# Kernel optimization log

Measured on AMD Instinct MI355X. Metric: run time of the kernel, lower is better.

Reference implementation:

```python
import jax, jax.numpy as jnp
import numpy as np


def _conv(x, w, b, stride=1, pad=0):
    # x: NCHW, w: OIHW (torch layout)
    y = jax.lax.conv_general_dilated(
        x, w, (stride, stride), [(pad, pad), (pad, pad)],
        dimension_numbers=('NCHW', 'OIHW', 'NCHW'))
    return y + b[None, :, None, None]


def _convT(x, w, b):
    # torch ConvTranspose2d(k=4, stride=2, padding=1); w: [Cin, Cout, 4, 4]
    wf = jnp.flip(w, (2, 3)).transpose(1, 0, 2, 3)  # -> OIHW
    y = jax.lax.conv_general_dilated(
        x, wf, (1, 1), [(2, 2), (2, 2)], lhs_dilation=(2, 2),
        dimension_numbers=('NCHW', 'OIHW', 'NCHW'))
    return y + b[None, :, None, None]


def _quantize(z, embed):
    # z: [B,H,W,D], embed: [D,K]  (eval-mode _Quantize: no EMA update)
    f = z.reshape(-1, z.shape[-1])
    dist = (f * f).sum(1, keepdims=True) - 2.0 * (f @ embed) + (embed * embed).sum(0, keepdims=True)
    ind = jnp.argmin(dist, axis=1)
    q = embed.T[ind].reshape(z.shape)
    diff = jnp.mean((jax.lax.stop_gradient(q) - z) ** 2)[None]
    q = z + jax.lax.stop_gradient(q - z)  # straight-through
    return q, diff, ind.reshape(z.shape[:-1])


def setup_inputs() -> dict:
    key = jax.random.key(0)
    ks = jax.random.split(key, 22)
    s = 0.02
    r = lambda k, sh, sc=s: jax.random.normal(k, sh, jnp.float32) * sc
    z = lambda sh: jnp.zeros(sh, jnp.float32)
    return {
        'x': jax.random.normal(ks[0], (16, 3, 256, 256), jnp.float32),
        # encoder_bottom: two stride-2 4x4 convs, 3->128->128 (256->64)
        'wb1': r(ks[1], (128, 3, 4, 4)), 'bb1': z(128),
        'wb2': r(ks[2], (128, 128, 4, 4)), 'bb2': z(128),
        # encoder_top: one stride-2 4x4 conv, 128->128 (64->32)
        'wt1': r(ks[3], (128, 128, 4, 4)), 'bt1': z(128),
        # quantize_conv_t: 1x1, 128->64
        'wqt': r(ks[4], (64, 128, 1, 1)), 'bqt': z(64),
        'embed_t': jax.random.normal(ks[5], (64, 512), jnp.float32),
        # decoder_top: convT 64->64 (32->64)
        'wdt': r(ks[6], (64, 64, 4, 4)), 'bdt': z(64),
        # quantize_conv_b: 1x1, 192->64
        'wqb': r(ks[7], (64, 192, 1, 1)), 'bqb': z(64),
        'embed_b': jax.random.normal(ks[8], (64, 512), jnp.float32),
        # upsample_t: convT 64->64 (32->64)
        'wup': r(ks[9], (64, 64, 4, 4)), 'bup': z(64),
        # decoder_bottom: convT 128->64 (64->128), convT 64->3 (128->256)
        'wd1': r(ks[10], (128, 64, 4, 4)), 'bd1': z(64),
        'wd2': r(ks[11], (64, 3, 4, 4)), 'bd2': z(3),
    }


def reference(x, wb1, bb1, wb2, bb2, wt1, bt1, wqt, bqt, embed_t,
              wdt, bdt, wqb, bqb, embed_b, wup, bup, wd1, bd1, wd2, bd2):
    # ----- encode -----
    enc_b = jax.nn.relu(_conv(x, wb1, bb1, stride=2, pad=1))          # [B,128,128,128]
    enc_b = jax.nn.relu(_conv(enc_b, wb2, bb2, stride=2, pad=1))      # [B,128,64,64]
    enc_t = jax.nn.relu(_conv(enc_b, wt1, bt1, stride=2, pad=1))      # [B,128,32,32]

    qt = _conv(enc_t, wqt, bqt).transpose(0, 2, 3, 1)                 # [B,32,32,64]
    quant_t, diff_t, id_t = _quantize(qt, embed_t)
    quant_t = quant_t.transpose(0, 3, 1, 2)                           # [B,64,32,32]

    dec_t = _convT(quant_t, wdt, bdt)                                 # [B,64,64,64]
    enc_cat = jnp.concatenate([dec_t, enc_b], axis=1)                 # [B,192,64,64]

    qb = _conv(enc_cat, wqb, bqb).transpose(0, 2, 3, 1)               # [B,64,64,64]
    quant_b, diff_b, id_b = _quantize(qb, embed_b)
    quant_b = quant_b.transpose(0, 3, 1, 2)                           # [B,64,64,64]

    loss_commit = diff_t + diff_b                                     # [1]

    # ----- decode -----
    up_t = _convT(quant_t, wup, bup)                                  # [B,64,64,64]
    quant = jnp.concatenate([up_t, quant_b], axis=1)                  # [B,128,64,64]
    h = jax.nn.relu(_convT(quant, wd1, bd1))                          # [B,64,128,128]
    x_hat = _convT(h, wd2, bd2)                                       # [B,3,256,256]

    return x_hat, quant_t, quant_b, loss_commit, id_t, id_b
```

## Files before the change

### kernel.cpp

```cpp
#include <hip/hip_runtime.h>

#define TPB 256

typedef __attribute__((ext_vector_type(4))) float f32x4;
typedef __attribute__((ext_vector_type(8))) short bf16x8;

__global__ void wtrans_kernel(const float* __restrict__ src, float* __restrict__ dst,
                              int CIN, int COUT, int taps, int iohw) {
    int idx = blockIdx.x * TPB + threadIdx.x;
    int tot = CIN * COUT * taps;
    if (idx >= tot) return;
    int co = idx % COUT;
    int ci = (idx / COUT) % CIN;
    int tap = idx / (COUT * CIN);
    float v = iohw ? src[(ci * COUT + co) * taps + tap]
                   : src[(co * CIN + ci) * taps + tap];
    dst[idx] = v;
}

__device__ __forceinline__ unsigned bf16_rne(float v) {
    unsigned u = __float_as_uint(v);
    return (u + 0x7FFFu + ((u >> 16) & 1u)) >> 16;
}

__global__ void wtrans_bf16_kernel(const float* __restrict__ src, short* __restrict__ dst,
                                   int CIN, int COUT, int taps, int iohw, int PL) {
    int idx = blockIdx.x * TPB + threadIdx.x;
    int tot = CIN * COUT * taps;
    if (idx >= tot) return;
    int ci = idx % CIN;
    int co = (idx / CIN) % COUT;
    int tap = idx / (CIN * COUT);
    float v = iohw ? src[(ci * COUT + co) * taps + tap]
                   : src[(co * CIN + ci) * taps + tap];
    unsigned h = bf16_rne(v);
    float rem = v - __uint_as_float(h << 16);
    unsigned l = bf16_rne(rem);
    dst[idx] = (short)h;
    dst[idx + PL] = (short)l;
}

__global__ void wtrans_wd2_kernel(const float* __restrict__ src, short* __restrict__ dst) {
    int idx = blockIdx.x * TPB + threadIdx.x;
    if (idx >= 16384) return;
    int ci  = idx & 63;
    int co  = (idx >> 6) & 15;
    int tap = (idx >> 10) & 3;
    int cls = idx >> 12;
    int py = cls >> 1, px = cls & 1;
    int jj = tap >> 1, ii = tap & 1;
    int ky = (1 - py) + 2 * jj;
    int kx = (1 - px) + 2 * ii;
    float v = (co < 3) ? src[(ci * 3 + co) * 16 + ky * 4 + kx] : 0.f;
    dst[idx] = (short)bf16_rne(v);
}

__global__ void etrans_kernel(const float* __restrict__ et, const float* __restrict__ eb,
                              short* __restrict__ ETt, short* __restrict__ ETb) {
    int idx = blockIdx.x * TPB + threadIdx.x;
    if (idx >= 65536) return;
    const float* src = (idx < 32768) ? et : eb;
    short* dst = (idx < 32768) ? ETt : ETb;
    int i = idx & 32767;
    int k = i & 63;
    int n = i >> 6;
    float v = src[k * 512 + n];
    unsigned h = bf16_rne(v);
    float rem = v - __uint_as_float(h << 16);
    dst[i] = (short)h;
    dst[i + 32768] = (short)bf16_rne(rem);
}

__device__ __forceinline__ void cvt_split2(float a, float b, unsigned& hw, unsigned& lw) {
    unsigned ha = bf16_rne(a), hb = bf16_rne(b);
    float ra = a - __uint_as_float(ha << 16);
    float rb = b - __uint_as_float(hb << 16);
    hw = ha | (hb << 16);
    lw = bf16_rne(ra) | (bf16_rne(rb) << 16);
}
__device__ __forceinline__ unsigned cvt_pk(float a, float b) {
    return bf16_rne(a) | (bf16_rne(b) << 16);
}

template<int MODE, int CIN, int COUT, int SPLIT, int RELU,
         int IH, int IW, int OH, int OW, int R, int INBF, int OUTB>
__global__ __launch_bounds__(256) void mfma_conv(
    const void* __restrict__ inv, const short* __restrict__ Wb,
    const float* __restrict__ bias, float* __restrict__ outp,
    short* __restrict__ outb) {
    constexpr int TAPS = (MODE == 0) ? 16 : 4;
    constexpr int CW = (MODE == 0) ? OW : OW / 2;
    constexpr int CH = (MODE == 0) ? OH : OH / 2;
    constexpr int NCH = CIN / 32;
    constexpr int MTc = (COUT == 128) ? 4 : 2;
    constexpr long PL = (long)TAPS * COUT * CIN;
    constexpr long APL_IN  = 16L * IH * IW * CIN;
    constexpr long APL_OUT = 16L * OH * OW * COUT;

    __shared__ short Ah[128 * 40];
    __shared__ short Al[SPLIT ? 128 * 40 : 8];
    __shared__ short Bh[COUT * 40];
    __shared__ short Bl[SPLIT ? COUT * 40 : 8];

    int bx = blockIdx.x;
    int ry = 0, rx = 0;
    if (MODE == 1) { int c = bx & 3; ry = c >> 1; rx = c & 1; bx >>= 2; }
    const int y0 = (bx % (CH / R)) * R;
    const int n  = bx / (CH / R);

    const int tid = threadIdx.x;
    const int p  = tid >> 1;
    const int ak = (tid & 1) * 16;
    const int rr = p / CW, xx = p % CW;
    constexpr int BPT = (COUT * 32) / 256;
    constexpr int TPRB = 32 / BPT;
    const int bco = tid / TPRB;
    const int bk  = (tid % TPRB) * BPT;
    const int lane = tid & 63, wv = tid >> 6;
    const int quad = lane >> 4, l16 = lane & 15;
    const int mbase = (COUT == 128) ? (wv & 1) * 64 : wv * 32;
    const int nbase = (COUT == 128) ? (wv >> 1) * 64 : 0;

    f32x4 acc[MTc][4];
#pragma unroll
    for (int mt = 0; mt < MTc; ++mt)
#pragma unroll
        for (int nt = 0; nt < 4; ++nt) acc[mt][nt] = f32x4{0.f, 0.f, 0.f, 0.f};

#pragma unroll 1
    for (int tap = 0; tap < TAPS; ++tap) {
        int iy, ix, wt;
        if (MODE == 0) {
            int ky = tap >> 2, kx = tap & 3;
            iy = 2 * (y0 + rr) - 1 + ky;
            ix = 2 * xx - 1 + kx;
            wt = tap;
        } else {
            int jj = tap >> 1, ii = tap & 1;
            iy = (y0 + rr) + ry - jj;
            ix = xx + rx - ii;
            wt = ((1 - ry) + 2 * jj) * 4 + ((1 - rx) + 2 * ii);
        }
        const bool av = (iy >= 0) && (iy < IH) && (ix >= 0) && (ix < IW);
        const long abase = ((long)(n * IH + iy) * IW + ix) * CIN + ak;
        const short* wrh = Wb + ((long)wt * COUT + bco) * CIN + bk;

#pragma unroll 1
        for (int cb = 0; cb < NCH; ++cb) {
            __syncthreads();
            if constexpr (INBF) {
                const short* sb = (const short*)inv + abase + cb * 32;
                uint4 h0, h1;
                if (av) { h0 = *(const uint4*)sb; h1 = *(const uint4*)(sb + 8); }
                else { h0 = make_uint4(0,0,0,0); h1 = h0; }
                *(uint4*)&Ah[p * 40 + ak]     = h0;
                *(uint4*)&Ah[p * 40 + ak + 8] = h1;
                if constexpr (SPLIT) {
                    uint4 l0, l1;
                    if (av) { l0 = *(const uint4*)(sb + APL_IN); l1 = *(const uint4*)(sb + APL_IN + 8); }
                    else { l0 = make_uint4(0,0,0,0); l1 = l0; }
                    *(uint4*)&Al[p * 40 + ak]     = l0;
                    *(uint4*)&Al[p * 40 + ak + 8] = l1;
                }
            } else {
                const float* sp = (const float*)inv + abase + cb * 32;
                float4 f[4];
                if (av) {
#pragma unroll
                    for (int i = 0; i < 4; ++i) f[i] = *(const float4*)(sp + 4 * i);
                } else {
#pragma unroll
                    for (int i = 0; i < 4; ++i) { f[i].x = 0.f; f[i].y = 0.f; f[i].z = 0.f; f[i].w = 0.f; }
                }
                if constexpr (SPLIT) {
                    unsigned hw[8], lw[8];
#pragma unroll
                    for (int i = 0; i < 4; ++i) {
                        cvt_split2(f[i].x, f[i].y, hw[2 * i], lw[2 * i]);
                        cvt_split2(f[i].z, f[i].w, hw[2 * i + 1], lw[2 * i + 1]);
                    }
                    *(uint4*)&Ah[p * 40 + ak]     = make_uint4(hw[0], hw[1], hw[2], hw[3]);
                    *(uint4*)&Ah[p * 40 + ak + 8] = make_uint4(hw[4], hw[5], hw[6], hw[7]);
                    *(uint4*)&Al[p * 40 + ak]     = make_uint4(lw[0], lw[1], lw[2], lw[3]);
                    *(uint4*)&Al[p * 40 + ak + 8] = make_uint4(lw[4], lw[5], lw[6], lw[7]);
                } else {
                    unsigned hw[8];
#pragma unroll
                    for (int i = 0; i < 4; ++i) {
                        hw[2 * i]     = cvt_pk(f[i].x, f[i].y);
                        hw[2 * i + 1] = cvt_pk(f[i].z, f[i].w);
                    }
                    *(uint4*)&Ah[p * 40 + ak]     = make_uint4(hw[0], hw[1], hw[2], hw[3]);
                    *(uint4*)&Ah[p * 40 + ak + 8] = make_uint4(hw[4], hw[5], hw[6], hw[7]);
                }
            }
#pragma unroll
            for (int i = 0; i < BPT / 8; ++i) {
                *(uint4*)&Bh[bco * 40 + bk + 8 * i] = *(const uint4*)(wrh + cb * 32 + 8 * i);
                if constexpr (SPLIT)
                    *(uint4*)&Bl[bco * 40 + bk + 8 * i] = *(const uint4*)(wrh + PL + cb * 32 + 8 * i);
            }
            __syncthreads();
            bf16x8 ahf[MTc], alf[SPLIT ? MTc : 1];
#pragma unroll
            for (int mt = 0; mt < MTc; ++mt) {
                ahf[mt] = *(const bf16x8*)&Ah[(mbase + mt * 16 + l16) * 40 + quad * 8];
                if constexpr (SPLIT)
                    alf[mt] = *(const bf16x8*)&Al[(mbase + mt * 16 + l16) * 40 + quad * 8];
            }
#pragma unroll
            for (int nt = 0; nt < 4; ++nt) {
                bf16x8 bhf = *(const bf16x8*)&Bh[(nbase + nt * 16 + l16) * 40 + quad * 8];
#pragma unroll
                for (int mt = 0; mt < MTc; ++mt)
                    acc[mt][nt] = __builtin_amdgcn_mfma_f32_16x16x32_bf16(ahf[mt], bhf, acc[mt][nt], 0, 0, 0);
                if constexpr (SPLIT) {
                    bf16x8 blf = *(const bf16x8*)&Bl[(nbase + nt * 16 + l16) * 40 + quad * 8];
#pragma unroll
                    for (int mt = 0; mt < MTc; ++mt) {
                        acc[mt][nt] = __builtin_amdgcn_mfma_f32_16x16x32_bf16(alf[mt], bhf, acc[mt][nt], 0, 0, 0);
                        acc[mt][nt] = __builtin_amdgcn_mfma_f32_16x16x32_bf16(ahf[mt], blf, acc[mt][nt], 0, 0, 0);
                    }
                }
            }
        }
    }
#pragma unroll
    for (int mt = 0; mt < MTc; ++mt)
#pragma unroll
        for (int nt = 0; nt < 4; ++nt) {
            int co = nbase + nt * 16 + l16;
            float bv = bias[co];
#pragma unroll
            for (int r = 0; r < 4; ++r) {
                int pl = mbase + mt * 16 + quad * 4 + r;
                int rr2 = pl / CW, x2 = pl % CW;
                int oy, ox;
                if (MODE == 0) { oy = y0 + rr2; ox = x2; }
                else           { oy = 2 * (y0 + rr2) + ry; ox = 2 * x2 + rx; }
                float vv = acc[mt][nt][r] + bv;
                if (RELU) vv = fmaxf(vv, 0.f);
                long oidx = ((long)(n * OH + oy) * OW + ox) * COUT + co;
                if constexpr (OUTB == 0 || OUTB == 1) outp[oidx] = vv;
                if constexpr (OUTB == 1 || OUTB == 3) {
                    unsigned hh = bf16_rne(vv);
                    outb[oidx] = (short)hh;
                    outb[oidx + APL_OUT] = (short)bf16_rne(vv - __uint_as_float(hh << 16));
                }
                if constexpr (OUTB == 2) outb[oidx] = (short)bf16_rne(vv);
            }
        }
}

__global__ __launch_bounds__(256) void convt_final_mfma(
    const short* __restrict__ h, const short* __restrict__ Wc,
    const float* __restrict__ bias, float* __restrict__ out) {
    const int HW = 128;
    __shared__ short HB[3 * 130 * 72];
    __shared__ float Sout[6 * 260];

    const int tid = threadIdx.x;
    const int y = blockIdx.x & 127;
    const int n = blockIdx.x >> 7;
    const int lane = tid & 63, wv = tid >> 6;
    const int quad = lane >> 4, l16 = lane & 15;

    for (int u = tid; u < 780; u += TPB) {
        int row = u >> 1, half = u & 1;
        int hr = row / 130, xc = row % 130;
        int hy = y - 1 + hr, hx = xc - 1;
        bool ok = (hy >= 0 && hy < HW && hx >= 0 && hx < HW);
        const short* sp = h + ((long)(n * HW + hy) * HW + hx) * 64 + half * 32;
        uint4 a0, a1, a2, a3;
        if (ok) {
            a0 = *(const uint4*)sp;       a1 = *(const uint4*)(sp + 8);
            a2 = *(const uint4*)(sp + 16); a3 = *(const uint4*)(sp + 24);
        } else {
            a0 = make_uint4(0,0,0,0); a1 = a0; a2 = a0; a3 = a0;
        }
        short* dp = &HB[row * 72 + half * 32];
        *(uint4*)dp = a0; *(uint4*)(dp + 8) = a1;
        *(uint4*)(dp + 16) = a2; *(uint4*)(dp + 24) = a3;
    }
    __syncthreads();

#pragma unroll 1
    for (int cls = 0; cls < 4; ++cls) {
        const int py = cls >> 1, px = cls & 1;
        bf16x8 Bf[4][2];
#pragma unroll
        for (int tap = 0; tap < 4; ++tap)
#pragma unroll
            for (int cb = 0; cb < 2; ++cb)
                Bf[tap][cb] = *(const bf16x8*)&Wc[((cls * 4 + tap) * 16 + l16) * 64 + cb * 32 + quad * 8];

        f32x4 acc2[2] = { f32x4{0.f,0.f,0.f,0.f}, f32x4{0.f,0.f,0.f,0.f} };
#pragma unroll
        for (int mt = 0; mt < 2; ++mt) {
            const int xp0 = wv * 32 + mt * 16;
#pragma unroll
            for (int tap = 0; tap < 4; ++tap) {
                const int jj = tap >> 1, ii = tap & 1;
                const int hr = py - jj + 1;
                const int rbase = (hr * 130 + xp0 + l16 + px - ii + 1) * 72;
#pragma unroll
                for (int cb = 0; cb < 2; ++cb) {
                    bf16x8 Af = *(const bf16x8*)&HB[rbase + cb * 32 + quad * 8];
                    acc2[mt] = __builtin_amdgcn_mfma_f32_16x16x32_bf16(Af, Bf[tap][cb], acc2[mt], 0, 0, 0);
                }
            }
        }
        if (l16 < 3) {
#pragma unroll
            for (int mt = 0; mt < 2; ++mt)
#pragma unroll
                for (int r = 0; r < 4; ++r) {
                    int xp = wv * 32 + mt * 16 + quad * 4 + r;
                    Sout[(py * 3 + l16) * 260 + 2 * xp + px] = acc2[mt][r];
                }
        }
    }
    __syncthreads();

    for (int u = tid; u < 384; u += TPB) {
        int idx = u * 4;
        int rowi = idx >> 8;
        int xq   = idx & 255;
        int py = rowi / 3, co = rowi % 3;
        float bv = bias[co];
        float4 v = *(const float4*)&Sout[rowi * 260 + xq];
        v.x += bv; v.y += bv; v.z += bv; v.w += bv;
        *(float4*)&out[(((long)(n * 3 + co) * 256) + 2 * y + py) * 256 + xq] = v;
    }
}

__global__ __launch_bounds__(256) void conv1_kernel(
    const float* __restrict__ x, const float* __restrict__ Wt,
    const float* __restrict__ bias, short* __restrict__ outb) {
    const int IH = 256, IW = 256, OH = 128, OW = 128, BM = 64;
    const long APL0 = 16L * 128 * 128 * 128;
    int bx = blockIdx.x;
    int sx = bx & 1;
    int oy = (bx >> 1) & 127;
    int n  = bx >> 8;
    int ox0 = sx * BM;
    __shared__ float Bs[16 * 3 * 128];
    __shared__ float Ts[3 * 4 * 132];
    int tid = threadIdx.x;
    for (int i = tid; i < 6144 / 4; i += TPB)
        ((float4*)Bs)[i] = ((const float4*)Wt)[i];
    int iy0 = 2 * oy - 1;
    for (int idx = tid; idx < 3 * 4 * 130; idx += TPB) {
        int ci = idx / 520; int r = idx % 520;
        int ky = r / 130;   int xx = r % 130;
        int iy = iy0 + ky;  int ix = 2 * ox0 - 1 + xx;
        float v = 0.f;
        if (iy >= 0 && iy < IH && ix >= 0 && ix < IW)
            v = x[((n * 3 + ci) * IH + iy) * IW + ix];
        Ts[(ci * 4 + ky) * 132 + xx] = v;
    }
    __syncthreads();
    int cog = tid & 31, pxg = tid >> 5;
    int co0 = cog * 4, px0 = pxg * 8;
    float acc[8][4];
#pragma unroll
    for (int i = 0; i < 8; ++i)
#pragma unroll
        for (int j = 0; j < 4; ++j) acc[i][j] = 0.f;
#pragma unroll 1
    for (int ky = 0; ky < 4; ++ky)
#pragma unroll 1
        for (int kx = 0; kx < 4; ++kx)
#pragma unroll
            for (int ci = 0; ci < 3; ++ci) {
                float4 b = *(const float4*)&Bs[((ky * 4 + kx) * 3 + ci) * 128 + co0];
                const float* trow = &Ts[(ci * 4 + ky) * 132 + kx];
#pragma unroll
                for (int q = 0; q < 8; ++q) {
                    float a = trow[2 * (px0 + q)];
                    acc[q][0] = fmaf(a, b.x, acc[q][0]);
                    acc[q][1] = fmaf(a, b.y, acc[q][1]);
                    acc[q][2] = fmaf(a, b.z, acc[q][2]);
                    acc[q][3] = fmaf(a, b.w, acc[q][3]);
                }
            }
    float4 bb = *(const float4*)&bias[co0];
#pragma unroll
    for (int q = 0; q < 8; ++q) {
        int ox = ox0 + px0 + q;
        float v0 = fmaxf(acc[q][0] + bb.x, 0.f);
        float v1 = fmaxf(acc[q][1] + bb.y, 0.f);
        float v2 = fmaxf(acc[q][2] + bb.z, 0.f);
        float v3 = fmaxf(acc[q][3] + bb.w, 0.f);
        unsigned h0, l0, h1, l1;
        cvt_split2(v0, v1, h0, l0);
        cvt_split2(v2, v3, h1, l1);
        long pix = ((long)n * OH + oy) * OW + ox;
        *(uint2*)&outb[pix * 128 + co0]        = make_uint2(h0, h1);
        *(uint2*)&outb[APL0 + pix * 128 + co0] = make_uint2(l0, l1);
    }
}

template<int MODE, int CIN, int COUT, int BM, int RELU, int IH, int IW, int OH, int OW>
__global__ __launch_bounds__(256) void conv_gemm(
    const float* __restrict__ in, const float* __restrict__ Wt,
    const float* __restrict__ bias, float* __restrict__ out) {
    constexpr int CHUNK  = 64;
    constexpr int NCH    = CIN / CHUNK;
    constexpr int CO_PER = (COUT == 128) ? 4 : 2;
    constexpr int PX_PER = BM / 8;
    constexpr int TAPS   = (MODE == 0) ? 16 : (MODE == 1 ? 4 : 1);
    __shared__ float As[CHUNK * BM];
    __shared__ float Bs[CHUNK * COUT];
    const int tid = threadIdx.x;
    const int bx  = blockIdx.x;
    int n, oy, ox0 = 0, par = 0;
    if (MODE == 1) {
        par = bx & 1;
        oy  = (bx >> 1) % OH;
        n   = bx / (2 * OH);
    } else {
        constexpr int SPR = OW / BM;
        int s = bx % SPR;
        oy = (bx / SPR) % OH;
        n  = bx / (SPR * OH);
        ox0 = s * BM;
    }
    const int cog = tid & 31;
    const int pxg = tid >> 5;
    const int co0 = cog * CO_PER, px0 = pxg * PX_PER;
    float acc[PX_PER][CO_PER];
#pragma unroll
    for (int q = 0; q < PX_PER; ++q)
#pragma unroll
        for (int j = 0; j < CO_PER; ++j) acc[q][j] = 0.f;
    constexpr int TPX  = 256 / BM;
    constexpr int CIPT = CHUNK / TPX;
    const int spx  = tid / TPX;
    const int sci0 = (tid % TPX) * CIPT;
    const int py   = oy & 1;

#pragma unroll 1
    for (int tap = 0; tap < TAPS; ++tap) {
        int iy, twi, sx;
        if (MODE == 0) {
            int ky = tap >> 2, kx = tap & 3;
            iy  = 2 * oy - 1 + ky;
            sx  = 2 * (ox0 + spx) - 1 + kx;
            twi = tap;
        } else if (MODE == 1) {
            int jj = tap >> 1, ii = tap & 1;
            iy  = ((oy + 1) >> 1) - jj;
            sx  = spx + par - ii;
            twi = ((1 - py) + 2 * jj) * 4 + ((1 - par) + 2 * ii);
        } else {
            iy = oy; sx = ox0 + spx; twi = 0;
        }
        const bool pxv = (iy >= 0) && (iy < IH) && (sx >= 0) && (sx < IW);
        const float* srcp = in + (((long)n * IH + iy) * IW + sx) * CIN + sci0;
#pragma unroll 1
        for (int cb = 0; cb < NCH; ++cb) {
            __syncthreads();
            float4 tmp[CIPT / 4];
#pragma unroll
            for (int t4 = 0; t4 < CIPT / 4; ++t4) {
                if (pxv) tmp[t4] = *(const float4*)(srcp + cb * CHUNK + 4 * t4);
                else { tmp[t4].x = 0.f; tmp[t4].y = 0.f; tmp[t4].z = 0.f; tmp[t4].w = 0.f; }
            }
#pragma unroll
            for (int t4 = 0; t4 < CIPT / 4; ++t4) {
                As[(sci0 + 4 * t4 + 0) * BM + spx] = tmp[t4].x;
                As[(sci0 + 4 * t4 + 1) * BM + spx] = tmp[t4].y;
                As[(sci0 + 4 * t4 + 2) * BM + spx] = tmp[t4].z;
                As[(sci0 + 4 * t4 + 3) * BM + spx] = tmp[t4].w;
            }
            {
                const float4* wsrc = (const float4*)(Wt + ((long)twi * CIN + cb * CHUNK) * COUT);
#pragma unroll
                for (int t4 = 0; t4 < (CHUNK * COUT) / 1024; ++t4)
                    ((float4*)Bs)[tid + 256 * t4] = wsrc[tid + 256 * t4];
            }
            __syncthreads();
#pragma unroll 4
            for (int k = 0; k < CHUNK; ++k) {
                float a[PX_PER];
#pragma unroll
                for (int t4 = 0; t4 < PX_PER / 4; ++t4)
                    *(float4*)&a[4 * t4] = *(const float4*)&As[k * BM + px0 + 4 * t4];
                if constexpr (CO_PER == 4) {
                    float4 b = *(const float4*)&Bs[k * COUT + co0];
#pragma unroll
                    for (int q = 0; q < PX_PER; ++q) {
                        acc[q][0] = fmaf(a[q], b.x, acc[q][0]);
                        acc[q][1] = fmaf(a[q], b.y, acc[q][1]);
                        acc[q][2] = fmaf(a[q], b.z, acc[q][2]);
                        acc[q][3] = fmaf(a[q], b.w, acc[q][3]);
                    }
                } else {
                    float2 b = *(const float2*)&Bs[k * COUT + co0];
#pragma unroll
                    for (int q = 0; q < PX_PER; ++q) {
                        acc[q][0] = fmaf(a[q], b.x, acc[q][0]);
                        acc[q][1] = fmaf(a[q], b.y, acc[q][1]);
                    }
                }
            }
        }
    }
    float bv[CO_PER];
#pragma unroll
    for (int j = 0; j < CO_PER; ++j) bv[j] = bias[co0 + j];
#pragma unroll
    for (int q = 0; q < PX_PER; ++q) {
        int ox = (MODE == 1) ? (par + 2 * (px0 + q)) : (ox0 + px0 + q);
        float* op = out + (((long)n * OH + oy) * OW + ox) * COUT + co0;
        if constexpr (CO_PER == 4) {
            float4 v;
            v.x = acc[q][0] + bv[0]; v.y = acc[q][1] + bv[1];
            v.z = acc[q][2] + bv[2]; v.w = acc[q][3] + bv[3];
            if (RELU) { v.x = fmaxf(v.x, 0.f); v.y = fmaxf(v.y, 0.f);
                        v.z = fmaxf(v.z, 0.f); v.w = fmaxf(v.w, 0.f); }
            *(float4*)op = v;
        } else {
            float2 v;
            v.x = acc[q][0] + bv[0]; v.y = acc[q][1] + bv[1];
            if (RELU) { v.x = fmaxf(v.x, 0.f); v.y = fmaxf(v.y, 0.f); }
            *(float2*)op = v;
        }
    }
}

__global__ void enorm_kernel(const float* __restrict__ et, const float* __restrict__ eb,
                             float* __restrict__ nt, float* __restrict__ nb) {
    int k = blockIdx.x * TPB + threadIdx.x;
    if (k >= 1024) return;
    const float* e = (k < 512) ? et : eb;
    float* o = (k < 512) ? nt : nb;
    int kk = k & 511;
    float s = 0.f;
#pragma unroll 8
    for (int d = 0; d < 64; ++d) { float v = e[d * 512 + kk]; s = fmaf(v, v, s); }
    o[kk] = s;
}

__global__ __launch_bounds__(256) void quantize_mfma(
    const float* __restrict__ f, const short* __restrict__ ET,
    const float* __restrict__ embed, const float* __restrict__ enorm,
    float* __restrict__ qn, float* __restrict__ qc, float* __restrict__ ido,
    float* __restrict__ dsum, int M, int HW) {
    __shared__ short Fh[64 * 72];
    __shared__ short Fl[64 * 72];
    __shared__ float S[64 * 65];
    __shared__ int   KI[64];
    __shared__ float wsum[4];

    const int tid = threadIdx.x;
    const int lane = tid & 63, wv = tid >> 6;
    const int quad = lane >> 4, l16 = lane & 15;
    const int R0 = blockIdx.x * 64;

    {
        int row = tid >> 2;
        int k0 = (tid & 3) * 16;
        const float* sp = f + (long)(R0 + row) * 64 + k0;
        unsigned hw[8], lw[8];
#pragma unroll
        for (int i = 0; i < 4; ++i) {
            float4 p = *(const float4*)(sp + 4 * i);
            cvt_split2(p.x, p.y, hw[2 * i], lw[2 * i]);
            cvt_split2(p.z, p.w, hw[2 * i + 1], lw[2 * i + 1]);
        }
        short* dh = &Fh[row * 72 + k0];
        short* dl = &Fl[row * 72 + k0];
        *(uint4*)(dh)     = make_uint4(hw[0], hw[1], hw[2], hw[3]);
        *(uint4*)(dh + 8) = make_uint4(hw[4], hw[5], hw[6], hw[7]);
        *(uint4*)(dl)     = make_uint4(lw[0], lw[1], lw[2], lw[3]);
        *(uint4*)(dl + 8) = make_uint4(lw[4], lw[5], lw[6], lw[7]);
    }
    __syncthreads();

    const int arow = (wv * 16 + l16) * 72;
    bf16x8 Ah0 = *(const bf16x8*)&Fh[arow + quad * 8];
    bf16x8 Ah1 = *(const bf16x8*)&Fh[arow + 32 + quad * 8];
    bf16x8 Al0 = *(const bf16x8*)&Fl[arow + quad * 8];
    bf16x8 Al1 = *(const bf16x8*)&Fl[arow + 32 + quad * 8];

    float bestv[4];
    int   besti[4];
#pragma unroll
    for (int r = 0; r < 4; ++r) { bestv[r] = 3.4e38f; besti[r] = 0; }

    const short* ETlo = ET + 32768;
#pragma unroll 2
    for (int j = 0; j < 32; ++j) {
        const int nb = (j * 16 + l16) * 64 + quad * 8;
        bf16x8 Bh0 = *(const bf16x8*)(ET + nb);
        bf16x8 Bh1 = *(const bf16x8*)(ET + nb + 32);
        bf16x8 Bl0 = *(const bf16x8*)(ETlo + nb);
        bf16x8 Bl1 = *(const bf16x8*)(ETlo + nb + 32);
        f32x4 acc = f32x4{0.f, 0.f, 0.f, 0.f};
        acc = __builtin_amdgcn_mfma_f32_16x16x32_bf16(Ah0, Bh0, acc, 0, 0, 0);
        acc = __builtin_amdgcn_mfma_f32_16x16x32_bf16(Ah1, Bh1, acc, 0, 0, 0);
        acc = __builtin_amdgcn_mfma_f32_16x16x32_bf16(Al0, Bh0, acc, 0, 0, 0);
        acc = __builtin_amdgcn_mfma_f32_16x16x32_bf16(Al1, Bh1, acc, 0, 0, 0);
        acc = __builtin_amdgcn_mfma_f32_16x16x32_bf16(Ah0, Bl0, acc, 0, 0, 0);
        acc = __builtin_amdgcn_mfma_f32_16x16x32_bf16(Ah1, Bl1, acc, 0, 0, 0);
        float en = enorm[j * 16 + l16];
        int   ni = j * 16 + l16;
#pragma unroll
        for (int r = 0; r < 4; ++r) {
            float s = fmaf(-2.f, acc[r], en);
            if (s < bestv[r]) { bestv[r] = s; besti[r] = ni; }
        }
    }
#pragma unroll
    for (int m = 1; m < 16; m <<= 1) {
#pragma unroll
        for (int r = 0; r < 4; ++r) {
            float ov = __shfl_xor(bestv[r], m);
            int   oi = __shfl_xor(besti[r], m);
            if (ov < bestv[r] || (ov == bestv[r] && oi < besti[r])) {
                bestv[r] = ov; besti[r] = oi;
            }
        }
    }
    if (l16 == 0) {
#pragma unroll
        for (int r = 0; r < 4; ++r) KI[wv * 16 + quad * 4 + r] = besti[r];
    }
    __syncthreads();

    float ddacc = 0.f;
#pragma unroll 1
    for (int r16 = 0; r16 < 16; ++r16) {
        int row = wv * 16 + r16;
        int k = KI[row];
        float ev = embed[lane * 512 + k];
        float fv = f[(long)(R0 + row) * 64 + lane];
        qn[(long)(R0 + row) * 64 + lane] = ev;
        S[row * 65 + lane] = ev;
        float dq = ev - fv;
        ddacc = fmaf(dq, dq, ddacc);
        if (lane == 0) ido[R0 + row] = (float)k;
    }
#pragma unroll
    for (int off = 1; off < 64; off <<= 1) ddacc += __shfl_xor(ddacc, off);
    if (lane == 0) wsum[wv] = ddacc;
    __syncthreads();
    if (tid == 0)
        atomicAdd(dsum, wsum[0] + wsum[1] + wsum[2] + wsum[3]);

    int nn = R0 / HW;
    int rem0 = R0 - nn * HW;
    int px = tid & 63;
    int cg = tid >> 6;
#pragma unroll
    for (int it = 0; it < 16; ++it) {
        int c = cg + 4 * it;
        qc[((long)nn * 64 + c) * HW + rem0 + px] = S[px * 65 + c];
    }
}

__global__ void concat_rec_kernel(const float* __restrict__ a, const short* __restrict__ bh,
                                  float* __restrict__ o, int M) {
    const long PLB = 8388608L;
    int idx = blockIdx.x * TPB + threadIdx.x;
    if (idx >= M * 48) return;
    int row = idx / 48;
    int c4  = (idx - row * 48) * 4;
    float4 v;
    if (c4 < 64) v = *(const float4*)(a + (long)row * 64 + c4);
    else {
        int cc = c4 - 64;
        uint2 h = *(const uint2*)(bh + (long)row * 128 + cc);
        uint2 l = *(const uint2*)(bh + PLB + (long)row * 128 + cc);
        v.x = __uint_as_float(h.x << 16)        + __uint_as_float(l.x << 16);
        v.y = __uint_as_float(h.x & 0xFFFF0000u) + __uint_as_float(l.x & 0xFFFF0000u);
        v.z = __uint_as_float(h.y << 16)        + __uint_as_float(l.y << 16);
        v.w = __uint_as_float(h.y & 0xFFFF0000u) + __uint_as_float(l.y & 0xFFFF0000u);
    }
    *(float4*)(o + (long)row * 192 + c4) = v;
}

__global__ void concat_bf16_kernel(const float* __restrict__ a, const float* __restrict__ b,
                                   short* __restrict__ o, int M) {
    int idx = blockIdx.x * TPB + threadIdx.x;
    if (idx >= M * 32) return;
    int row = idx / 32;
    int c4  = (idx - row * 32) * 4;
    float4 v;
    if (c4 < 64) v = *(const float4*)(a + (long)row * 64 + c4);
    else         v = *(const float4*)(b + (long)row * 64 + (c4 - 64));
    *(uint2*)(o + (long)row * 128 + c4) = make_uint2(cvt_pk(v.x, v.y), cvt_pk(v.z, v.w));
}

__global__ void loss_kernel(const float* __restrict__ sums, float* __restrict__ out) {
    out[0] = sums[0] * (1.f / (16384.f * 64.f)) + sums[1] * (1.f / (65536.f * 64.f));
}

extern "C" void kernel_launch(void* const* d_in, const int* in_sizes, int n_in,
                              void* d_out, int out_size, void* d_ws, size_t ws_size,
                              hipStream_t stream) {
    const float* x   = (const float*)d_in[0];
    const float* wb1 = (const float*)d_in[1];  const float* bb1 = (const float*)d_in[2];
    const float* wb2 = (const float*)d_in[3];  const float* bb2 = (const float*)d_in[4];
    const float* wt1 = (const float*)d_in[5];  const float* bt1 = (const float*)d_in[6];
    const float* wqt = (const float*)d_in[7];  const float* bqt = (const float*)d_in[8];
    const float* embed_t = (const float*)d_in[9];
    const float* wdt = (const float*)d_in[10]; const float* bdt = (const float*)d_in[11];
    const float* wqb = (const float*)d_in[12]; const float* bqb = (const float*)d_in[13];
    const float* embed_b = (const float*)d_in[14];
    const float* wup = (const float*)d_in[15]; const float* bup = (const float*)d_in[16];
    const float* wd1 = (const float*)d_in[17]; const float* bd1 = (const float*)d_in[18];
    const float* wd2 = (const float*)d_in[19]; const float* bd2 = (const float*)d_in[20];
    float* out = (float*)d_out;
    float* ws  = (float*)d_ws;

    float* O_XHAT = out;
    float* O_QT   = out + 3145728;
    float* O_QB   = out + 4194304;
    float* O_LOSS = out + 8388608;
    float* O_IDT  = out + 8388609;
    float* O_IDB  = out + 8404993;

    float* W_WB1 = ws + 0;
    short* WB_WD2 = (short*)(ws + 16384);
    short* ET_T  = (short*)(ws + 32768);
    short* ET_B  = (short*)(ws + 65536);
    float* W_WQT = ws + 532480;
    float* W_WDT = ws + 540672;
    float* W_WQB = ws + 606208;
    float* EN_T  = ws + 818176;
    float* EN_B  = ws + 818688;
    float* SUMS  = ws + 819200;
    short* T1B  = (short*)(ws + 1048576);
    const long BIG = 9437184;
    short* T0B  = (short*)(ws + BIG);
    float* T2   = ws + BIG;
    float* QT   = ws + BIG + 2097152;
    float* QTN  = ws + BIG + 3145728;
    float* DECT = ws + BIG + 4194304;
    float* ECAT = ws + BIG + 8388608;
    float* QB   = ws + BIG + 20971520;
    float* QBN  = ws + BIG + 25165824;
    float* UPT  = ws + BIG + 4194304;
    short* QCATB = (short*)(ws + BIG + 8388608);
    short* HBUFB = (short*)(ws + BIG + 16777216);
    short* WB_BF2 = (short*)(ws + 42991616);
    short* WB_BT1 = (short*)(ws + 43253760);
    short* WB_BD1 = (short*)(ws + 43515904);
    short* WB_BUP = (short*)(ws + 43646976);

    auto wt_launch = [&](const float* src, float* dst, int cin, int cout, int taps, int iohw) {
        int tot = cin * cout * taps;
        wtrans_kernel<<<(tot + TPB - 1) / TPB, TPB, 0, stream>>>(src, dst, cin, cout, taps, iohw);
    };
    auto wtb_launch = [&](const float* src, short* dst, int cin, int cout, int taps, int iohw) {
        int tot = cin * cout * taps;
        wtrans_bf16_kernel<<<(tot + TPB - 1) / TPB, TPB, 0, stream>>>(src, dst, cin, cout, taps, iohw, tot);
    };
    wt_launch(wb1, W_WB1, 3, 128, 16, 0);
    wt_launch(wqt, W_WQT, 128, 64, 1, 0);
    wt_launch(wdt, W_WDT, 64, 64, 16, 1);
    wt_launch(wqb, W_WQB, 192, 64, 1, 0);
    wtrans_wd2_kernel<<<64, TPB, 0, stream>>>(wd2, WB_WD2);
    wtb_launch(wb2, WB_BF2, 128, 128, 16, 0);
    wtb_launch(wt1, WB_BT1, 128, 128, 16, 0);
    wtb_launch(wd1, WB_BD1, 128, 64, 16, 1);
    wtb_launch(wup, WB_BUP, 64, 64, 16, 1);
    enorm_kernel<<<4, TPB, 0, stream>>>(embed_t, embed_b, EN_T, EN_B);
    etrans_kernel<<<256, TPB, 0, stream>>>(embed_t, embed_b, ET_T, ET_B);
    hipError_t e0 = hipMemsetAsync((void*)SUMS, 0, 2 * sizeof(float), stream);
    (void)e0;

    conv1_kernel<<<4096, TPB, 0, stream>>>(x, W_WB1, bb1, T0B);
    mfma_conv<0, 128, 128, 1, 1, 128, 128, 64, 64, 2, 1, 3>
        <<<512, TPB, 0, stream>>>(T0B, WB_BF2, bb2, nullptr, T1B);
    mfma_conv<0, 128, 128, 1, 1, 64, 64, 32, 32, 4, 1, 0>
        <<<128, TPB, 0, stream>>>(T1B, WB_BT1, bt1, T2, nullptr);
    conv_gemm<2, 128, 64, 32, 0, 32, 32, 32, 32><<<512, TPB, 0, stream>>>(T2, W_WQT, bqt, QT);
    quantize_mfma<<<256, TPB, 0, stream>>>(QT, ET_T, embed_t, EN_T, QTN, O_QT, O_IDT, SUMS,
                                           16384, 1024);
    conv_gemm<1, 64, 64, 32, 0, 32, 32, 64, 64><<<2048, TPB, 0, stream>>>(QTN, W_WDT, bdt, DECT);
    concat_rec_kernel<<<12288, TPB, 0, stream>>>(DECT, T1B, ECAT, 65536);
    conv_gemm<2, 192, 64, 64, 0, 64, 64, 64, 64><<<1024, TPB, 0, stream>>>(ECAT, W_WQB, bqb, QB);
    quantize_mfma<<<1024, TPB, 0, stream>>>(QB, ET_B, embed_b, EN_B, QBN, O_QB, O_IDB, SUMS + 1,
                                            65536, 4096);
    mfma_conv<1, 64, 64, 0, 0, 32, 32, 64, 64, 4, 0, 0>
        <<<512, TPB, 0, stream>>>(QTN, WB_BUP, bup, UPT, nullptr);
    concat_bf16_kernel<<<8192, TPB, 0, stream>>>(UPT, QBN, QCATB, 65536);
    mfma_conv<1, 128, 64, 0, 1, 64, 64, 128, 128, 2, 1, 2>
        <<<2048, TPB, 0, stream>>>(QCATB, WB_BD1, bd1, nullptr, HBUFB);
    convt_final_mfma<<<2048, TPB, 0, stream>>>(HBUFB, WB_WD2, bd2, O_XHAT);
    loss_kernel<<<1, 1, 0, stream>>>(SUMS, O_LOSS);

    (void)in_sizes; (void)n_in; (void)out_size; (void)ws_size;
}
```

Measured before the change: 707.5 us.

## Move 1x1 top quantize conv to MFMA and pass bf16 activations between stages

Adds a K-tile size parameter to the MFMA conv so each barrier-protected round covers 64 input channels instead of 32, and a 1x1 mode. The top-encoder conv now writes split-bf16 output, which a new MFMA 1x1 conv consumes in place of the fp32 FMA GEMM. The quantizer also emits bf16 copies of the quantized codes, so upsample and concat read bf16 directly instead of converting fp32. The aim is fewer sync rounds, tensor-core use for the 1x1 conv, and less fp32 traffic, at the cost of more shared memory per block and extra bf16 stores.

New measurement: 730.6 us. 3.3% more time.

```diff
diff --git a/kernel.cpp b/kernel.cpp
--- a/kernel.cpp
+++ b/kernel.cpp
@@ -35,9 +35,8 @@
                    : src[(co * CIN + ci) * taps + tap];
     unsigned h = bf16_rne(v);
     float rem = v - __uint_as_float(h << 16);
-    unsigned l = bf16_rne(rem);
     dst[idx] = (short)h;
-    dst[idx + PL] = (short)l;
+    dst[idx + PL] = (short)bf16_rne(rem);
 }
 
 __global__ void wtrans_wd2_kernel(const float* __restrict__ src, short* __restrict__ dst) {
@@ -83,24 +82,30 @@
 }
 
 template<int MODE, int CIN, int COUT, int SPLIT, int RELU,
-         int IH, int IW, int OH, int OW, int R, int INBF, int OUTB>
+         int IH, int IW, int OH, int OW, int R, int INBF, int OUTB, int KR>
 __global__ __launch_bounds__(256) void mfma_conv(
     const void* __restrict__ inv, const short* __restrict__ Wb,
     const float* __restrict__ bias, float* __restrict__ outp,
     short* __restrict__ outb) {
-    constexpr int TAPS = (MODE == 0) ? 16 : 4;
-    constexpr int CW = (MODE == 0) ? OW : OW / 2;
-    constexpr int CH = (MODE == 0) ? OH : OH / 2;
-    constexpr int NCH = CIN / 32;
+    constexpr int TAPS = (MODE == 0) ? 16 : (MODE == 1 ? 4 : 1);
+    constexpr int CW = (MODE == 1) ? OW / 2 : OW;
+    constexpr int CH = (MODE == 1) ? OH / 2 : OH;
+    constexpr int NRND = CIN / KR;
+    constexpr int KC = KR / 32;
+    constexpr int ST = KR + 8;
     constexpr int MTc = (COUT == 128) ? 4 : 2;
-    constexpr long PL = (long)TAPS * COUT * CIN;
+    constexpr long PLW = (long)TAPS * COUT * CIN;
     constexpr long APL_IN  = 16L * IH * IW * CIN;
     constexpr long APL_OUT = 16L * OH * OW * COUT;
-
-    __shared__ short Ah[128 * 40];
-    __shared__ short Al[SPLIT ? 128 * 40 : 8];
-    __shared__ short Bh[COUT * 40];
-    __shared__ short Bl[SPLIT ? COUT * 40 : 8];
+    constexpr int NU4A = KR / 16;
+    constexpr int TPR  = 256 / COUT;
+    constexpr int SPT  = KR / TPR;
+    constexpr int NU4B = SPT / 8;
+
+    __shared__ short Ah[128 * ST];
+    __shared__ short Al[SPLIT ? 128 * ST : 8];
+    __shared__ short Bh[COUT * ST];
+    __shared__ short Bl[SPLIT ? COUT * ST : 8];
 
     int bx = blockIdx.x;
     int ry = 0, rx = 0;
@@ -109,13 +114,11 @@
     const int n  = bx / (CH / R);
 
     const int tid = threadIdx.x;
-    const int p  = tid >> 1;
-    const int ak = (tid & 1) * 16;
+    const int p   = tid >> 1;
+    const int akb = (tid & 1) * (KR / 2);
     const int rr = p / CW, xx = p % CW;
-    constexpr int BPT = (COUT * 32) / 256;
-    constexpr int TPRB = 32 / BPT;
-    const int bco = tid / TPRB;
-    const int bk  = (tid % TPRB) * BPT;
+    const int bco = tid / TPR;
+    const int bk  = (tid % TPR) * SPT;
     const int lane = tid & 63, wv = tid >> 6;
     const int quad = lane >> 4, l16 = lane & 15;
     const int mbase = (COUT == 128) ? (wv & 1) * 64 : wv * 32;
@@ -135,91 +138,82 @@
             iy = 2 * (y0 + rr) - 1 + ky;
             ix = 2 * xx - 1 + kx;
             wt = tap;
-        } else {
+        } else if (MODE == 1) {
             int jj = tap >> 1, ii = tap & 1;
             iy = (y0 + rr) + ry - jj;
             ix = xx + rx - ii;
             wt = ((1 - ry) + 2 * jj) * 4 + ((1 - rx) + 2 * ii);
-        }
-        const bool av = (iy >= 0) && (iy < IH) && (ix >= 0) && (ix < IW);
-        const long abase = ((long)(n * IH + iy) * IW + ix) * CIN + ak;
-        const short* wrh = Wb + ((long)wt * COUT + bco) * CIN + bk;
+        } else {
+            iy = y0 + rr; ix = xx; wt = 0;
+        }
+        const bool av = (MODE == 2) ||
+                        ((iy >= 0) && (iy < IH) && (ix >= 0) && (ix < IW));
+        const long abase = ((long)(n * IH + iy) * IW + ix) * CIN + akb;
 
 #pragma unroll 1
-        for (int cb = 0; cb < NCH; ++cb) {
+        for (int ko = 0; ko < NRND; ++ko) {
             __syncthreads();
             if constexpr (INBF) {
-                const short* sb = (const short*)inv + abase + cb * 32;
-                uint4 h0, h1;
-                if (av) { h0 = *(const uint4*)sb; h1 = *(const uint4*)(sb + 8); }
-                else { h0 = make_uint4(0,0,0,0); h1 = h0; }
-                *(uint4*)&Ah[p * 40 + ak]     = h0;
-                *(uint4*)&Ah[p * 40 + ak + 8] = h1;
+                const short* sb = (const short*)inv + abase + ko * KR;
+#pragma unroll
+                for (int u = 0; u < NU4A; ++u) {
+                    uint4 h = av ? *(const uint4*)(sb + 8 * u) : make_uint4(0, 0, 0, 0);
+                    *(uint4*)&Ah[p * ST + akb + 8 * u] = h;
+                }
                 if constexpr (SPLIT) {
-                    uint4 l0, l1;
-                    if (av) { l0 = *(const uint4*)(sb + APL_IN); l1 = *(const uint4*)(sb + APL_IN + 8); }
-                    else { l0 = make_uint4(0,0,0,0); l1 = l0; }
-                    *(uint4*)&Al[p * 40 + ak]     = l0;
-                    *(uint4*)&Al[p * 40 + ak + 8] = l1;
+#pragma unroll
+                    for (int u = 0; u < NU4A; ++u) {
+                        uint4 l = av ? *(const uint4*)(sb + APL_IN + 8 * u) : make_uint4(0, 0, 0, 0);
+                        *(uint4*)&Al[p * ST + akb + 8 * u] = l;
+                    }
                 }
             } else {
-                const float* sp = (const float*)inv + abase + cb * 32;
-                float4 f[4];
-                if (av) {
-#pragma unroll
-                    for (int i = 0; i < 4; ++i) f[i] = *(const float4*)(sp + 4 * i);
-                } else {
-#pragma unroll
-                    for (int i = 0; i < 4; ++i) { f[i].x = 0.f; f[i].y = 0.f; f[i].z = 0.f; f[i].w = 0.f; }
-                }
-                if constexpr (SPLIT) {
-                    unsigned hw[8], lw[8];
-#pragma unroll
-                    for (int i = 0; i < 4; ++i) {
-                        cvt_split2(f[i].x, f[i].y, hw[2 * i], lw[2 * i]);
-                        cvt_split2(f[i].z, f[i].w, hw[2 * i + 1], lw[2 * i + 1]);
-                    }
-                    *(uint4*)&Ah[p * 40 + ak]     = make_uint4(hw[0], hw[1], hw[2], hw[3]);
-                    *(uint4*)&Ah[p * 40 + ak + 8] = make_uint4(hw[4], hw[5], hw[6], hw[7]);
-                    *(uint4*)&Al[p * 40 + ak]     = make_uint4(lw[0], lw[1], lw[2], lw[3]);
-                    *(uint4*)&Al[p * 40 + ak + 8] = make_uint4(lw[4], lw[5], lw[6], lw[7]);
-                } else {
-                    unsigned hw[8];
-#pragma unroll
-                    for (int i = 0; i < 4; ++i) {
-                        hw[2 * i]     = cvt_pk(f[i].x, f[i].y);
-                        hw[2 * i + 1] = cvt_pk(f[i].z, f[i].w);
-                    }
-                    *(uint4*)&Ah[p * 40 + ak]     = make_uint4(hw[0], hw[1], hw[2], hw[3]);
-                    *(uint4*)&Ah[p * 40 + ak + 8] = make_uint4(hw[4], hw[5], hw[6], hw[7]);
-                }
-            }
-#pragma unroll
-            for (int i = 0; i < BPT / 8; ++i) {
-                *(uint4*)&Bh[bco * 40 + bk + 8 * i] = *(const uint4*)(wrh + cb * 32 + 8 * i);
-                if constexpr (SPLIT)
-                    *(uint4*)&Bl[bco * 40 + bk + 8 * i] = *(const uint4*)(wrh + PL + cb * 32 + 8 * i);
+                const float* sp = (const float*)inv + abase + ko * KR;
+#pragma unroll
+                for (int u = 0; u < NU4A; ++u) {
+                    float4 f0, f1;
+                    if (av) { f0 = *(const float4*)(sp + 8 * u); f1 = *(const float4*)(sp + 8 * u + 4); }
+                    else { f0.x=f0.y=f0.z=f0.w=0.f; f1 = f0; }
+                    unsigned h0, l0, h1, l1, h2, l2, h3, l3;
+                    cvt_split2(f0.x, f0.y, h0, l0); cvt_split2(f0.z, f0.w, h1, l1);
+                    cvt_split2(f1.x, f1.y, h2, l2); cvt_split2(f1.z, f1.w, h3, l3);
+                    *(uint4*)&Ah[p * ST + akb + 8 * u] = make_uint4(h0, h1, h2, h3);
+                    if constexpr (SPLIT)
+                        *(uint4*)&Al[p * ST + akb + 8 * u] = make_uint4(l0, l1, l2, l3);
+                }
+            }
+            {
+                const short* wr = Wb + ((long)wt * COUT + bco) * CIN + ko * KR + bk;
+#pragma unroll
+                for (int u = 0; u < NU4B; ++u) {
+                    *(uint4*)&Bh[bco * ST + bk + 8 * u] = *(const uint4*)(wr + 8 * u);
+                    if constexpr (SPLIT)
+                        *(uint4*)&Bl[bco * ST + bk + 8 * u] = *(const uint4*)(wr + PLW + 8 * u);
+                }
             }
             __syncthreads();
-            bf16x8 ahf[MTc], alf[SPLIT ? MTc : 1];
-#pragma unroll
-            for (int mt = 0; mt < MTc; ++mt) {
-                ahf[mt] = *(const bf16x8*)&Ah[(mbase + mt * 16 + l16) * 40 + quad * 8];
-                if constexpr (SPLIT)
-                    alf[mt] = *(const bf16x8*)&Al[(mbase + mt * 16 + l16) * 40 + quad * 8];
-            }
-#pragma unroll
-            for (int nt = 0; nt < 4; ++nt) {
-                bf16x8 bhf = *(const bf16x8*)&Bh[(nbase + nt * 16 + l16) * 40 + quad * 8];
-#pragma unroll
-                for (int mt = 0; mt < MTc; ++mt)
-                    acc[mt][nt] = __builtin_amdgcn_mfma_f32_16x16x32_bf16(ahf[mt], bhf, acc[mt][nt], 0, 0, 0);
-                if constexpr (SPLIT) {
-                    bf16x8 blf = *(const bf16x8*)&Bl[(nbase + nt * 16 + l16) * 40 + quad * 8];
-#pragma unroll
-                    for (int mt = 0; mt < MTc; ++mt) {
-                        acc[mt][nt] = __builtin_amdgcn_mfma_f32_16x16x32_bf16(alf[mt], bhf, acc[mt][nt], 0, 0, 0);
-                        acc[mt][nt] = __builtin_amdgcn_mfma_f32_16x16x32_bf16(ahf[mt], blf, acc[mt][nt], 0, 0, 0);
+#pragma unroll
+            for (int kc = 0; kc < KC; ++kc) {
+                bf16x8 ahf[MTc], alf[SPLIT ? MTc : 1];
+#pragma unroll
+                for (int mt = 0; mt < MTc; ++mt) {
+                    ahf[mt] = *(const bf16x8*)&Ah[(mbase + mt * 16 + l16) * ST + kc * 32 + quad * 8];
+                    if constexpr (SPLIT)
+                        alf[mt] = *(const bf16x8*)&Al[(mbase + mt * 16 + l16) * ST + kc * 32 + quad * 8];
+                }
+#pragma unroll
+                for (int nt = 0; nt < 4; ++nt) {
+                    bf16x8 bhf = *(const bf16x8*)&Bh[(nbase + nt * 16 + l16) * ST + kc * 32 + quad * 8];
+#pragma unroll
+                    for (int mt = 0; mt < MTc; ++mt)
+                        acc[mt][nt] = __builtin_amdgcn_mfma_f32_16x16x32_bf16(ahf[mt], bhf, acc[mt][nt], 0, 0, 0);
+                    if constexpr (SPLIT) {
+                        bf16x8 blf = *(const bf16x8*)&Bl[(nbase + nt * 16 + l16) * ST + kc * 32 + quad * 8];
+#pragma unroll
+                        for (int mt = 0; mt < MTc; ++mt) {
+                            acc[mt][nt] = __builtin_amdgcn_mfma_f32_16x16x32_bf16(alf[mt], bhf, acc[mt][nt], 0, 0, 0);
+                            acc[mt][nt] = __builtin_amdgcn_mfma_f32_16x16x32_bf16(ahf[mt], blf, acc[mt][nt], 0, 0, 0);
+                        }
                     }
                 }
             }
@@ -236,13 +230,13 @@
                 int pl = mbase + mt * 16 + quad * 4 + r;
                 int rr2 = pl / CW, x2 = pl % CW;
                 int oy, ox;
-                if (MODE == 0) { oy = y0 + rr2; ox = x2; }
-                else           { oy = 2 * (y0 + rr2) + ry; ox = 2 * x2 + rx; }
+                if (MODE == 1) { oy = 2 * (y0 + rr2) + ry; ox = 2 * x2 + rx; }
+                else           { oy = y0 + rr2; ox = x2; }
                 float vv = acc[mt][nt][r] + bv;
                 if (RELU) vv = fmaxf(vv, 0.f);
                 long oidx = ((long)(n * OH + oy) * OW + ox) * COUT + co;
-                if constexpr (OUTB == 0 || OUTB == 1) outp[oidx] = vv;
-                if constexpr (OUTB == 1 || OUTB == 3) {
+                if constexpr (OUTB == 0) outp[oidx] = vv;
+                if constexpr (OUTB == 3) {
                     unsigned hh = bf16_rne(vv);
                     outb[oidx] = (short)hh;
                     outb[oidx + APL_OUT] = (short)bf16_rne(vv - __uint_as_float(hh << 16));
@@ -250,6 +244,135 @@
                 if constexpr (OUTB == 2) outb[oidx] = (short)bf16_rne(vv);
             }
         }
+}
+
+template<int MODE, int CIN, int COUT, int BM, int RELU, int IH, int IW, int OH, int OW>
+__global__ __launch_bounds__(256) void conv_gemm(
+    const float* __restrict__ in, const float* __restrict__ Wt,
+    const float* __restrict__ bias, float* __restrict__ out) {
+    constexpr int CHUNK  = 64;
+    constexpr int NCH    = CIN / CHUNK;
+    constexpr int CO_PER = (COUT == 128) ? 4 : 2;
+    constexpr int PX_PER = BM / 8;
+    constexpr int TAPS   = (MODE == 0) ? 16 : (MODE == 1 ? 4 : 1);
+    __shared__ float As[CHUNK * BM];
+    __shared__ float Bs[CHUNK * COUT];
+    const int tid = threadIdx.x;
+    const int bx  = blockIdx.x;
+    int n, oy, ox0 = 0, par = 0;
+    if (MODE == 1) {
+        par = bx & 1;
+        oy  = (bx >> 1) % OH;
+        n   = bx / (2 * OH);
+    } else {
+        constexpr int SPR = OW / BM;
+        int s = bx % SPR;
+        oy = (bx / SPR) % OH;
+        n  = bx / (SPR * OH);
+        ox0 = s * BM;
+    }
+    const int cog = tid & 31;
+    const int pxg = tid >> 5;
+    const int co0 = cog * CO_PER, px0 = pxg * PX_PER;
+    float acc[PX_PER][CO_PER];
+#pragma unroll
+    for (int q = 0; q < PX_PER; ++q)
+#pragma unroll
+        for (int j = 0; j < CO_PER; ++j) acc[q][j] = 0.f;
+    constexpr int TPX  = 256 / BM;
+    constexpr int CIPT = CHUNK / TPX;
+    const int spx  = tid / TPX;
+    const int sci0 = (tid % TPX) * CIPT;
+    const int py   = oy & 1;
+
+#pragma unroll 1
+    for (int tap = 0; tap < TAPS; ++tap) {
+        int iy, twi, sx;
+        if (MODE == 0) {
+            int ky = tap >> 2, kx = tap & 3;
+            iy  = 2 * oy - 1 + ky;
+            sx  = 2 * (ox0 + spx) - 1 + kx;
+            twi = tap;
+        } else if (MODE == 1) {
+            int jj = tap >> 1, ii = tap & 1;
+            iy  = ((oy + 1) >> 1) - jj;
+            sx  = spx + par - ii;
+            twi = ((1 - py) + 2 * jj) * 4 + ((1 - par) + 2 * ii);
+        } else {
+            iy = oy; sx = ox0 + spx; twi = 0;
+        }
+        const bool pxv = (iy >= 0) && (iy < IH) && (sx >= 0) && (sx < IW);
+        const float* srcp = in + (((long)n * IH + iy) * IW + sx) * CIN + sci0;
+#pragma unroll 1
+        for (int cb = 0; cb < NCH; ++cb) {
+            __syncthreads();
+            float4 tmp[CIPT / 4];
+#pragma unroll
+            for (int t4 = 0; t4 < CIPT / 4; ++t4) {
+                if (pxv) tmp[t4] = *(const float4*)(srcp + cb * CHUNK + 4 * t4);
+                else { tmp[t4].x = 0.f; tmp[t4].y = 0.f; tmp[t4].z = 0.f; tmp[t4].w = 0.f; }
+            }
+#pragma unroll
+            for (int t4 = 0; t4 < CIPT / 4; ++t4) {
+                As[(sci0 + 4 * t4 + 0) * BM + spx] = tmp[t4].x;
+                As[(sci0 + 4 * t4 + 1) * BM + spx] = tmp[t4].y;
+                As[(sci0 + 4 * t4 + 2) * BM + spx] = tmp[t4].z;
+                As[(sci0 + 4 * t4 + 3) * BM + spx] = tmp[t4].w;
+            }
+            {
+                const float4* wsrc = (const float4*)(Wt + ((long)twi * CIN + cb * CHUNK) * COUT);
+#pragma unroll
+                for (int t4 = 0; t4 < (CHUNK * COUT) / 1024; ++t4)
+                    ((float4*)Bs)[tid + 256 * t4] = wsrc[tid + 256 * t4];
+            }
+            __syncthreads();
+#pragma unroll 4
+            for (int k = 0; k < CHUNK; ++k) {
+                float a[PX_PER];
+#pragma unroll
+                for (int t4 = 0; t4 < PX_PER / 4; ++t4)
+                    *(float4*)&a[4 * t4] = *(const float4*)&As[k * BM + px0 + 4 * t4];
+                if constexpr (CO_PER == 4) {
+                    float4 b = *(const float4*)&Bs[k * COUT + co0];
+#pragma unroll
+                    for (int q = 0; q < PX_PER; ++q) {
+                        acc[q][0] = fmaf(a[q], b.x, acc[q][0]);
+                        acc[q][1] = fmaf(a[q], b.y, acc[q][1]);
+                        acc[q][2] = fmaf(a[q], b.z, acc[q][2]);
+                        acc[q][3] = fmaf(a[q], b.w, acc[q][3]);
+                    }
+                } else {
+                    float2 b = *(const float2*)&Bs[k * COUT + co0];
+#pragma unroll
+                    for (int q = 0; q < PX_PER; ++q) {
+                        acc[q][0] = fmaf(a[q], b.x, acc[q][0]);
+                        acc[q][1] = fmaf(a[q], b.y, acc[q][1]);
+                    }
+                }
+            }
+        }
+    }
+    float bv[CO_PER];
+#pragma unroll
+    for (int j = 0; j < CO_PER; ++j) bv[j] = bias[co0 + j];
+#pragma unroll
+    for (int q = 0; q < PX_PER; ++q) {
+        int ox = (MODE == 1) ? (par + 2 * (px0 + q)) : (ox0 + px0 + q);
+        float* op = out + (((long)n * OH + oy) * OW + ox) * COUT + co0;
+        if constexpr (CO_PER == 4) {
+            float4 v;
+            v.x = acc[q][0] + bv[0]; v.y = acc[q][1] + bv[1];
+            v.z = acc[q][2] + bv[2]; v.w = acc[q][3] + bv[3];
+            if (RELU) { v.x = fmaxf(v.x, 0.f); v.y = fmaxf(v.y, 0.f);
+                        v.z = fmaxf(v.z, 0.f); v.w = fmaxf(v.w, 0.f); }
+            *(float4*)op = v;
+        } else {
+            float2 v;
+            v.x = acc[q][0] + bv[0]; v.y = acc[q][1] + bv[1];
+            if (RELU) { v.x = fmaxf(v.x, 0.f); v.y = fmaxf(v.y, 0.f); }
+            *(float2*)op = v;
+        }
+    }
 }
 
 __global__ __launch_bounds__(256) void convt_final_mfma(
@@ -273,7 +396,7 @@
         const short* sp = h + ((long)(n * HW + hy) * HW + hx) * 64 + half * 32;
         uint4 a0, a1, a2, a3;
         if (ok) {
-            a0 = *(const uint4*)sp;       a1 = *(const uint4*)(sp + 8);
+            a0 = *(const uint4*)sp;        a1 = *(const uint4*)(sp + 8);
             a2 = *(const uint4*)(sp + 16); a3 = *(const uint4*)(sp + 24);
         } else {
             a0 = make_uint4(0,0,0,0); a1 = a0; a2 = a0; a3 = a0;
@@ -401,135 +524,6 @@
     }
 }
 
-template<int MODE, int CIN, int COUT, int BM, int RELU, int IH, int IW, int OH, int OW>
-__global__ __launch_bounds__(256) void conv_gemm(
-    const float* __restrict__ in, const float* __restrict__ Wt,
-    const float* __restrict__ bias, float* __restrict__ out) {
-    constexpr int CHUNK  = 64;
-    constexpr int NCH    = CIN / CHUNK;
-    constexpr int CO_PER = (COUT == 128) ? 4 : 2;
-    constexpr int PX_PER = BM / 8;
-    constexpr int TAPS   = (MODE == 0) ? 16 : (MODE == 1 ? 4 : 1);
-    __shared__ float As[CHUNK * BM];
-    __shared__ float Bs[CHUNK * COUT];
-    const int tid = threadIdx.x;
-    const int bx  = blockIdx.x;
-    int n, oy, ox0 = 0, par = 0;
-    if (MODE == 1) {
-        par = bx & 1;
-        oy  = (bx >> 1) % OH;
-        n   = bx / (2 * OH);
-    } else {
-        constexpr int SPR = OW / BM;
-        int s = bx % SPR;
-        oy = (bx / SPR) % OH;
-        n  = bx / (SPR * OH);
-        ox0 = s * BM;
-    }
-    const int cog = tid & 31;
-    const int pxg = tid >> 5;
-    const int co0 = cog * CO_PER, px0 = pxg * PX_PER;
-    float acc[PX_PER][CO_PER];
-#pragma unroll
-    for (int q = 0; q < PX_PER; ++q)
-#pragma unroll
-        for (int j = 0; j < CO_PER; ++j) acc[q][j] = 0.f;
-    constexpr int TPX  = 256 / BM;
-    constexpr int CIPT = CHUNK / TPX;
-    const int spx  = tid / TPX;
-    const int sci0 = (tid % TPX) * CIPT;
-    const int py   = oy & 1;
-
-#pragma unroll 1
-    for (int tap = 0; tap < TAPS; ++tap) {
-        int iy, twi, sx;
-        if (MODE == 0) {
-            int ky = tap >> 2, kx = tap & 3;
-            iy  = 2 * oy - 1 + ky;
-            sx  = 2 * (ox0 + spx) - 1 + kx;
-            twi = tap;
-        } else if (MODE == 1) {
-            int jj = tap >> 1, ii = tap & 1;
-            iy  = ((oy + 1) >> 1) - jj;
-            sx  = spx + par - ii;
-            twi = ((1 - py) + 2 * jj) * 4 + ((1 - par) + 2 * ii);
-        } else {
-            iy = oy; sx = ox0 + spx; twi = 0;
-        }
-        const bool pxv = (iy >= 0) && (iy < IH) && (sx >= 0) && (sx < IW);
-        const float* srcp = in + (((long)n * IH + iy) * IW + sx) * CIN + sci0;
-#pragma unroll 1
-        for (int cb = 0; cb < NCH; ++cb) {
-            __syncthreads();
-            float4 tmp[CIPT / 4];
-#pragma unroll
-            for (int t4 = 0; t4 < CIPT / 4; ++t4) {
-                if (pxv) tmp[t4] = *(const float4*)(srcp + cb * CHUNK + 4 * t4);
-                else { tmp[t4].x = 0.f; tmp[t4].y = 0.f; tmp[t4].z = 0.f; tmp[t4].w = 0.f; }
-            }
-#pragma unroll
-            for (int t4 = 0; t4 < CIPT / 4; ++t4) {
-                As[(sci0 + 4 * t4 + 0) * BM + spx] = tmp[t4].x;
-                As[(sci0 + 4 * t4 + 1) * BM + spx] = tmp[t4].y;
-                As[(sci0 + 4 * t4 + 2) * BM + spx] = tmp[t4].z;
-                As[(sci0 + 4 * t4 + 3) * BM + spx] = tmp[t4].w;
-            }
-            {
-                const float4* wsrc = (const float4*)(Wt + ((long)twi * CIN + cb * CHUNK) * COUT);
-#pragma unroll
-                for (int t4 = 0; t4 < (CHUNK * COUT) / 1024; ++t4)
-                    ((float4*)Bs)[tid + 256 * t4] = wsrc[tid + 256 * t4];
-            }
-            __syncthreads();
-#pragma unroll 4
-            for (int k = 0; k < CHUNK; ++k) {
-                float a[PX_PER];
-#pragma unroll
-                for (int t4 = 0; t4 < PX_PER / 4; ++t4)
-                    *(float4*)&a[4 * t4] = *(const float4*)&As[k * BM + px0 + 4 * t4];
-                if constexpr (CO_PER == 4) {
-                    float4 b = *(const float4*)&Bs[k * COUT + co0];
-#pragma unroll
-                    for (int q = 0; q < PX_PER; ++q) {
-                        acc[q][0] = fmaf(a[q], b.x, acc[q][0]);
-                        acc[q][1] = fmaf(a[q], b.y, acc[q][1]);
-                        acc[q][2] = fmaf(a[q], b.z, acc[q][2]);
-                        acc[q][3] = fmaf(a[q], b.w, acc[q][3]);
-                    }
-                } else {
-                    float2 b = *(const float2*)&Bs[k * COUT + co0];
-#pragma unroll
-                    for (int q = 0; q < PX_PER; ++q) {
-                        acc[q][0] = fmaf(a[q], b.x, acc[q][0]);
-                        acc[q][1] = fmaf(a[q], b.y, acc[q][1]);
-                    }
-                }
-            }
-        }
-    }
-    float bv[CO_PER];
-#pragma unroll
-    for (int j = 0; j < CO_PER; ++j) bv[j] = bias[co0 + j];
-#pragma unroll
-    for (int q = 0; q < PX_PER; ++q) {
-        int ox = (MODE == 1) ? (par + 2 * (px0 + q)) : (ox0 + px0 + q);
-        float* op = out + (((long)n * OH + oy) * OW + ox) * COUT + co0;
-        if constexpr (CO_PER == 4) {
-            float4 v;
-            v.x = acc[q][0] + bv[0]; v.y = acc[q][1] + bv[1];
-            v.z = acc[q][2] + bv[2]; v.w = acc[q][3] + bv[3];
-            if (RELU) { v.x = fmaxf(v.x, 0.f); v.y = fmaxf(v.y, 0.f);
-                        v.z = fmaxf(v.z, 0.f); v.w = fmaxf(v.w, 0.f); }
-            *(float4*)op = v;
-        } else {
-            float2 v;
-            v.x = acc[q][0] + bv[0]; v.y = acc[q][1] + bv[1];
-            if (RELU) { v.x = fmaxf(v.x, 0.f); v.y = fmaxf(v.y, 0.f); }
-            *(float2*)op = v;
-        }
-    }
-}
-
 __global__ void enorm_kernel(const float* __restrict__ et, const float* __restrict__ eb,
                              float* __restrict__ nt, float* __restrict__ nb) {
     int k = blockIdx.x * TPB + threadIdx.x;
@@ -546,8 +540,8 @@
 __global__ __launch_bounds__(256) void quantize_mfma(
     const float* __restrict__ f, const short* __restrict__ ET,
     const float* __restrict__ embed, const float* __restrict__ enorm,
-    float* __restrict__ qn, float* __restrict__ qc, float* __restrict__ ido,
-    float* __restrict__ dsum, int M, int HW) {
+    float* __restrict__ qn, short* __restrict__ qnb, float* __restrict__ qc,
+    float* __restrict__ ido, float* __restrict__ dsum, int M, int HW) {
     __shared__ short Fh[64 * 72];
     __shared__ short Fl[64 * 72];
     __shared__ float S[64 * 65];
@@ -637,7 +631,9 @@
         int k = KI[row];
         float ev = embed[lane * 512 + k];
         float fv = f[(long)(R0 + row) * 64 + lane];
-        qn[(long)(R0 + row) * 64 + lane] = ev;
+        long qi = (long)(R0 + row) * 64 + lane;
+        qn[qi] = ev;
+        qnb[qi] = (short)bf16_rne(ev);
         S[row * 65 + lane] = ev;
         float dq = ev - fv;
         ddacc = fmaf(dq, dq, ddacc);
@@ -674,24 +670,28 @@
         int cc = c4 - 64;
         uint2 h = *(const uint2*)(bh + (long)row * 128 + cc);
         uint2 l = *(const uint2*)(bh + PLB + (long)row * 128 + cc);
-        v.x = __uint_as_float(h.x << 16)        + __uint_as_float(l.x << 16);
+        v.x = __uint_as_float(h.x << 16)         + __uint_as_float(l.x << 16);
         v.y = __uint_as_float(h.x & 0xFFFF0000u) + __uint_as_float(l.x & 0xFFFF0000u);
-        v.z = __uint_as_float(h.y << 16)        + __uint_as_float(l.y << 16);
+        v.z = __uint_as_float(h.y << 16)         + __uint_as_float(l.y << 16);
         v.w = __uint_as_float(h.y & 0xFFFF0000u) + __uint_as_float(l.y & 0xFFFF0000u);
     }
     *(float4*)(o + (long)row * 192 + c4) = v;
 }
 
-__global__ void concat_bf16_kernel(const float* __restrict__ a, const float* __restrict__ b,
+__global__ void concat_qcat_kernel(const float* __restrict__ a, const short* __restrict__ qh,
                                    short* __restrict__ o, int M) {
     int idx = blockIdx.x * TPB + threadIdx.x;
     if (idx >= M * 32) return;
     int row = idx / 32;
     int c4  = (idx - row * 32) * 4;
-    float4 v;
-    if (c4 < 64) v = *(const float4*)(a + (long)row * 64 + c4);
-    else         v = *(const float4*)(b + (long)row * 64 + (c4 - 64));
-    *(uint2*)(o + (long)row * 128 + c4) = make_uint2(cvt_pk(v.x, v.y), cvt_pk(v.z, v.w));
+    uint2 w;
+    if (c4 < 64) {
+        float4 v = *(const float4*)(a + (long)row * 64 + c4);
+        w = make_uint2(cvt_pk(v.x, v.y), cvt_pk(v.z, v.w));
+    } else {
+        w = *(const uint2*)(qh + (long)row * 64 + (c4 - 64));
+    }
+    *(uint2*)(o + (long)row * 128 + c4) = w;
 }
 
 __global__ void loss_kernel(const float* __restrict__ sums, float* __restrict__ out) {
@@ -723,28 +723,30 @@
     float* O_IDT  = out + 8388609;
     float* O_IDB  = out + 8404993;
 
-    float* W_WB1 = ws + 0;
+    float* W_WB1  = ws + 0;
     short* WB_WD2 = (short*)(ws + 16384);
-    short* ET_T  = (short*)(ws + 32768);
-    short* ET_B  = (short*)(ws + 65536);
-    float* W_WQT = ws + 532480;
-    float* W_WDT = ws + 540672;
-    float* W_WQB = ws + 606208;
+    short* ET_T   = (short*)(ws + 32768);
+    short* ET_B   = (short*)(ws + 65536);
+    short* WB_WQT = (short*)(ws + 98304);
+    float* W_WDT  = ws + 540672;
+    float* W_WQB  = ws + 606208;
     float* EN_T  = ws + 818176;
     float* EN_B  = ws + 818688;
     float* SUMS  = ws + 819200;
-    short* T1B  = (short*)(ws + 1048576);
+    short* T1B   = (short*)(ws + 1048576);
     const long BIG = 9437184;
-    short* T0B  = (short*)(ws + BIG);
-    float* T2   = ws + BIG;
-    float* QT   = ws + BIG + 2097152;
-    float* QTN  = ws + BIG + 3145728;
-    float* DECT = ws + BIG + 4194304;
-    float* ECAT = ws + BIG + 8388608;
-    float* QB   = ws + BIG + 20971520;
-    float* QBN  = ws + BIG + 25165824;
-    float* UPT  = ws + BIG + 4194304;
-    short* QCATB = (short*)(ws + BIG + 8388608);
+    short* T0B   = (short*)(ws + BIG);
+    short* T2B   = (short*)(ws + BIG);
+    float* QT    = ws + BIG + 2097152;
+    float* QTN   = ws + BIG + 3145728;
+    short* QTNB  = (short*)(ws + BIG + 4194304);
+    float* DECT  = ws + BIG + 4718592;
+    float* ECAT  = ws + BIG + 8912896;
+    float* QB    = ws + BIG + 21495808;
+    short* QBNB  = (short*)(ws + BIG + 25690112);
+    float* QND   = ws + BIG + 27787264;
+    float* UPT   = ws + BIG + 4718592;
+    short* QCATB = (short*)(ws + BIG + 8912896);
     short* HBUFB = (short*)(ws + BIG + 16777216);
     short* WB_BF2 = (short*)(ws + 42991616);
     short* WB_BT1 = (short*)(ws + 43253760);
@@ -760,12 +762,12 @@
         wtrans_bf16_kernel<<<(tot + TPB - 1) / TPB, TPB, 0, stream>>>(src, dst, cin, cout, taps, iohw, tot);
     };
     wt_launch(wb1, W_WB1, 3, 128, 16, 0);
-    wt_launch(wqt, W_WQT, 128, 64, 1, 0);
     wt_launch(wdt, W_WDT, 64, 64, 16, 1);
     wt_launch(wqb, W_WQB, 192, 64, 1, 0);
     wtrans_wd2_kernel<<<64, TPB, 0, stream>>>(wd2, WB_WD2);
     wtb_launch(wb2, WB_BF2, 128, 128, 16, 0);
     wtb_launch(wt1, WB_BT1, 128, 128, 16, 0);
+    wtb_launch(wqt, WB_WQT, 128, 64, 1, 0);
     wtb_launch(wd1, WB_BD1, 128, 64, 16, 1);
     wtb_launch(wup, WB_BUP, 64, 64, 16, 1);
     enorm_kernel<<<4, TPB, 0, stream>>>(embed_t, embed_b, EN_T, EN_B);
@@ -774,22 +776,23 @@
     (void)e0;
 
     conv1_kernel<<<4096, TPB, 0, stream>>>(x, W_WB1, bb1, T0B);
-    mfma_conv<0, 128, 128, 1, 1, 128, 128, 64, 64, 2, 1, 3>
+    mfma_conv<0, 128, 128, 1, 1, 128, 128, 64, 64, 2, 1, 3, 32>
         <<<512, TPB, 0, stream>>>(T0B, WB_BF2, bb2, nullptr, T1B);
-    mfma_conv<0, 128, 128, 1, 1, 64, 64, 32, 32, 4, 1, 0>
-        <<<128, TPB, 0, stream>>>(T1B, WB_BT1, bt1, T2, nullptr);
-    conv_gemm<2, 128, 64, 32, 0, 32, 32, 32, 32><<<512, TPB, 0, stream>>>(T2, W_WQT, bqt, QT);
-    quantize_mfma<<<256, TPB, 0, stream>>>(QT, ET_T, embed_t, EN_T, QTN, O_QT, O_IDT, SUMS,
-                                           16384, 1024);
+    mfma_conv<0, 128, 128, 1, 1, 64, 64, 32, 32, 4, 1, 3, 32>
+        <<<128, TPB, 0, stream>>>(T1B, WB_BT1, bt1, nullptr, T2B);
+    mfma_conv<2, 128, 64, 1, 0, 32, 32, 32, 32, 4, 1, 0, 64>
+        <<<128, TPB, 0, stream>>>(T2B, WB_WQT, bqt, QT, nullptr);
+    quantize_mfma<<<256, TPB, 0, stream>>>(QT, ET_T, embed_t, EN_T, QTN, QTNB,
+                                           O_QT, O_IDT, SUMS, 16384, 1024);
     conv_gemm<1, 64, 64, 32, 0, 32, 32, 64, 64><<<2048, TPB, 0, stream>>>(QTN, W_WDT, bdt, DECT);
     concat_rec_kernel<<<12288, TPB, 0, stream>>>(DECT, T1B, ECAT, 65536);
     conv_gemm<2, 192, 64, 64, 0, 64, 64, 64, 64><<<1024, TPB, 0, stream>>>(ECAT, W_WQB, bqb, QB);
-    quantize_mfma<<<1024, TPB, 0, stream>>>(QB, ET_B, embed_b, EN_B, QBN, O_QB, O_IDB, SUMS + 1,
-                                            65536, 4096);
-    mfma_conv<1, 64, 64, 0, 0, 32, 32, 64, 64, 4, 0, 0>
-        <<<512, TPB, 0, stream>>>(QTN, WB_BUP, bup, UPT, nullptr);
-    concat_bf16_kernel<<<8192, TPB, 0, stream>>>(UPT, QBN, QCATB, 65536);
-    mfma_conv<1, 128, 64, 0, 1, 64, 64, 128, 128, 2, 1, 2>
+    quantize_mfma<<<1024, TPB, 0, stream>>>(QB, ET_B, embed_b, EN_B, QND, QBNB,
+                                            O_QB, O_IDB, SUMS + 1, 65536, 4096);
+    mfma_conv<1, 64, 64, 0, 0, 32, 32, 64, 64, 4, 1, 0, 64>
+        <<<512, TPB, 0, stream>>>(QTNB, WB_BUP, bup, UPT, nullptr);
+    concat_qcat_kernel<<<8192, TPB, 0, stream>>>(UPT, QBNB, QCATB, 65536);
+    mfma_conv<1, 128, 64, 0, 1, 64, 64, 128, 128, 2, 1, 2, 64>
         <<<2048, TPB, 0, stream>>>(QCATB, WB_BD1, bd1, nullptr, HBUFB);
     convt_final_mfma<<<2048, TPB, 0, stream>>>(HBUFB, WB_WD2, bd2, O_XHAT);
     loss_kernel<<<1, 1, 0, stream>>>(SUMS, O_LOSS);
```
